# Kernel optimization log

Hardware: AMD Instinct MI355X
Metric: run time of the kernel (lower is better)

The kernel has to match this reference:

```python
import jax, jax.numpy as jnp
import numpy as np

B, T, C, H = 4, 1024, 1024, 16
HD = C // H
EPS = 1e-5


def _layernorm(x, w, b):
    mu = jnp.mean(x, axis=-1, keepdims=True)
    var = jnp.mean(jnp.square(x - mu), axis=-1, keepdims=True)
    return (x - mu) * jax.lax.rsqrt(var + EPS) * w + b


def setup_inputs() -> dict:
    key = jax.random.key(0)
    ks = jax.random.split(key, 10)
    s = 0.02
    return {
        "x": jax.random.normal(ks[0], (B, T, C), jnp.float32),
        "attention_mask": jnp.zeros((1, 1, T, T), jnp.float32),
        "ln1_w": jnp.ones((C,), jnp.float32),
        "ln1_b": jnp.zeros((C,), jnp.float32),
        "w_qkv": s * jax.random.normal(ks[1], (3 * C, C), jnp.float32),
        "b_qkv": jnp.zeros((3 * C,), jnp.float32),
        "w_o": s * jax.random.normal(ks[2], (C, C), jnp.float32),
        "b_o": jnp.zeros((C,), jnp.float32),
        "ln2_w": jnp.ones((C,), jnp.float32),
        "ln2_b": jnp.zeros((C,), jnp.float32),
        "w_fc": s * jax.random.normal(ks[3], (4 * C, C), jnp.float32),
        "b_fc": jnp.zeros((4 * C,), jnp.float32),
        "w_proj": s * jax.random.normal(ks[4], (C, 4 * C), jnp.float32),
        "b_proj": jnp.zeros((C,), jnp.float32),
    }


def reference(x, attention_mask, ln1_w, ln1_b, w_qkv, b_qkv, w_o, b_o,
              ln2_w, ln2_b, w_fc, b_fc, w_proj, b_proj):
    # --- self-attention on ln_1(x) ---
    h = _layernorm(x, ln1_w, ln1_b)
    qkv = h @ w_qkv.T + b_qkv                      # [B,T,3C]
    q, k, v = jnp.split(qkv, 3, axis=-1)
    q = q.reshape(B, T, H, HD).transpose(0, 2, 1, 3)  # [B,H,T,HD]
    k = k.reshape(B, T, H, HD).transpose(0, 2, 1, 3)
    v = v.reshape(B, T, H, HD).transpose(0, 2, 1, 3)
    att = jnp.einsum('bhqd,bhkd->bhqk', q, k) * (1.0 / np.sqrt(HD))
    att = att + attention_mask
    att_weights = jax.nn.softmax(att, axis=-1)     # [B,H,T,T]
    y = jnp.einsum('bhqk,bhkd->bhqd', att_weights, v)
    y = y.transpose(0, 2, 1, 3).reshape(B, T, C)
    y = y @ w_o.T + b_o
    x = x + y
    # --- MLP on ln_2(x), residual ---
    residual = x
    h2 = _layernorm(x, ln2_w, ln2_b)
    h2 = jax.nn.gelu(h2 @ w_fc.T + b_fc, approximate=False)
    h2 = h2 @ w_proj.T + b_proj
    x = residual + h2
    return (x, att_weights)
```

## Files before the change

### kernel.cpp

```cpp
#include <hip/hip_runtime.h>
#include <stdint.h>
#include <math.h>

typedef __attribute__((ext_vector_type(4))) float f32x4;
typedef __attribute__((ext_vector_type(8))) short s16x8;
typedef __attribute__((ext_vector_type(4))) unsigned short u16x4;
typedef __attribute__((ext_vector_type(8))) unsigned short u16x8;

__device__ __forceinline__ unsigned short f2b(float x) {
    union { float f; uint32_t u; } v; v.f = x;
    uint32_t r = v.u + 0x7FFFu + ((v.u >> 16) & 1u);
    return (unsigned short)(r >> 16);
}
__device__ __forceinline__ float b2f(unsigned short u) {
    union { uint32_t u; float f; } v; v.u = (uint32_t)u << 16;
    return v.f;
}

__device__ __forceinline__ void gload16(const unsigned short* g, unsigned short* l) {
    __builtin_amdgcn_global_load_lds(
        (const __attribute__((address_space(1))) unsigned int*)(const void*)g,
        (__attribute__((address_space(3))) unsigned int*)(void*)l,
        16, 0, 0);
}

__global__ __launch_bounds__(256) void cast4_kernel(
        const float* __restrict__ a, int na, const float* __restrict__ b, int nb,
        const float* __restrict__ c, int nc, const float* __restrict__ d, int nd,
        unsigned short* __restrict__ oa, unsigned short* __restrict__ ob,
        unsigned short* __restrict__ oc, unsigned short* __restrict__ od) {
    int i = blockIdx.x * 256 + threadIdx.x;
    const float* src; unsigned short* dst; int off;
    if (i < na)                { src = a; dst = oa; off = i; }
    else if (i < na+nb)        { src = b; dst = ob; off = i - na; }
    else if (i < na+nb+nc)     { src = c; dst = oc; off = i - na - nb; }
    else if (i < na+nb+nc+nd)  { src = d; dst = od; off = i - na - nb - nc; }
    else return;
    f32x4 v = ((const f32x4*)src)[off];
    u16x4 o;
    #pragma unroll
    for (int j = 0; j < 4; ++j) o[j] = f2b(v[j]);
    ((u16x4*)dst)[off] = o;
}

__global__ __launch_bounds__(256) void ln_kernel(const float* __restrict__ x,
                                                 const float* __restrict__ w,
                                                 const float* __restrict__ b,
                                                 unsigned short* __restrict__ out) {
    const long row = blockIdx.x;
    const int tid = threadIdx.x;
    f32x4 v = *(const f32x4*)(x + row * 1024 + tid * 4);
    float s  = v[0] + v[1] + v[2] + v[3];
    float sq = v[0]*v[0] + v[1]*v[1] + v[2]*v[2] + v[3]*v[3];
    #pragma unroll
    for (int off = 32; off; off >>= 1) {
        s  += __shfl_xor(s, off);
        sq += __shfl_xor(sq, off);
    }
    __shared__ float red[8];
    if ((tid & 63) == 0) { red[tid >> 6] = s; red[4 + (tid >> 6)] = sq; }
    __syncthreads();
    s  = red[0] + red[1] + red[2] + red[3];
    sq = red[4] + red[5] + red[6] + red[7];
    float mu  = s * (1.0f / 1024.0f);
    float var = sq * (1.0f / 1024.0f) - mu * mu;
    float rs  = rsqrtf(var + 1e-5f);
    f32x4 wv = *(const f32x4*)(w + tid * 4);
    f32x4 bv = *(const f32x4*)(b + tid * 4);
    u16x4 o;
    #pragma unroll
    for (int j = 0; j < 4; ++j) o[j] = f2b((v[j] - mu) * rs * wv[j] + bv[j]);
    *(u16x4*)(out + row * 1024 + tid * 4) = o;
}

__global__ __launch_bounds__(256) void inv_kernel(const float* __restrict__ psum,
                                                  float* __restrict__ invl) {
    const long r = blockIdx.x * 256 + threadIdx.x;
    const float* p = psum + (r << 4);
    f32x4 a = *(const f32x4*)p,       b = *(const f32x4*)(p + 4);
    f32x4 c = *(const f32x4*)(p + 8), d = *(const f32x4*)(p + 12);
    float s = (a[0]+a[1]+a[2]+a[3]) + (b[0]+b[1]+b[2]+b[3])
            + (c[0]+c[1]+c[2]+c[3]) + (d[0]+d[1]+d[2]+d[3]);
    invl[r] = 1.0f / s;
}

__global__ __launch_bounds__(256)
void pv_att(const unsigned short* __restrict__ E,
            const unsigned short* __restrict__ Vt,
            const float* __restrict__ invl,
            float* __restrict__ att,
            unsigned short* __restrict__ y) {
    __shared__ unsigned short ldsA[3][64 * 32];
    __shared__ unsigned short ldsB[3][64 * 32];
    const int tid = threadIdx.x, lane = tid & 63, wid = tid >> 6;
    const int wr = wid >> 1, wc = wid & 1;
    const int bh = blockIdx.y;
    const int q0 = blockIdx.x * 64;
    const int fr = lane & 15, fs = lane >> 4;

    const unsigned short* Ab = E + ((long)bh << 20) + (long)q0 * 1024;
    const unsigned short* Bb = Vt + ((long)bh << 16);

    const int e0  = wid * 512 + lane * 8;
    const int r0a = e0 >> 5, c0a = e0 & 31;
    const float il_a = invl[(bh << 10) + q0 + r0a];
    float* attRow = att + ((long)bh << 20) + (long)(q0 + r0a) * 1024 + c0a;

    f32x4 acc[2][2] = {};

#define PSTAGE(T, BUF)                                                        \
    {                                                                         \
        const int k0s = (T) << 5;                                             \
        gload16(Ab + k0s + (long)r0a * 1024 + c0a, &ldsA[BUF][wid * 512]);    \
        gload16(Bb + k0s + (long)r0a * 1024 + c0a, &ldsB[BUF][wid * 512]);    \
    }

    PSTAGE(0, 0);
    PSTAGE(1, 1);

    for (int t = 0; t < 32; ++t) {
        const int buf = t % 3;
        asm volatile("s_waitcnt vmcnt(4)" ::: "memory");
        __syncthreads();
        if (t + 2 < 32) PSTAGE(t + 2, (t + 2) % 3);

        {
            s16x8 ea = *(const s16x8*)&ldsA[buf][e0];
            f32x4 o0, o1;
            #pragma unroll
            for (int j = 0; j < 4; ++j) o0[j] = b2f((unsigned short)ea[j]) * il_a;
            #pragma unroll
            for (int j = 0; j < 4; ++j) o1[j] = b2f((unsigned short)ea[4 + j]) * il_a;
            *(f32x4*)(attRow + t * 32)     = o0;
            *(f32x4*)(attRow + t * 32 + 4) = o1;
        }

        s16x8 af[2], vb[2];
        #pragma unroll
        for (int m = 0; m < 2; ++m)
            af[m] = *(const s16x8*)&ldsA[buf][(wr * 32 + m * 16 + fr) * 32 + fs * 8];
        #pragma unroll
        for (int n = 0; n < 2; ++n)
            vb[n] = *(const s16x8*)&ldsB[buf][(wc * 32 + n * 16 + fr) * 32 + fs * 8];
        #pragma unroll
        for (int m = 0; m < 2; ++m)
            #pragma unroll
            for (int n = 0; n < 2; ++n)
                acc[m][n] = __builtin_amdgcn_mfma_f32_16x16x32_bf16(af[m], vb[n], acc[m][n], 0, 0, 0);
    }
#undef PSTAGE

    const int bb = bh >> 4, hh = bh & 15;
    #pragma unroll
    for (int m = 0; m < 2; ++m) {
        #pragma unroll
        for (int r = 0; r < 4; ++r) {
            const int trow = q0 + wr * 32 + m * 16 + fs * 4 + r;
            const float il = invl[(bh << 10) + trow];
            #pragma unroll
            for (int n = 0; n < 2; ++n) {
                const int c = hh * 64 + wc * 32 + n * 16 + fr;
                y[((long)(bb * 1024 + trow) << 10) + c] = f2b(acc[m][n][r] * il);
            }
        }
    }
}

template <int BM, int BN, int EPI>
__global__ __launch_bounds__(256)
void gemm_bt(const unsigned short* __restrict__ A,
             const unsigned short* __restrict__ Bm,
             int K, int lda, int ldb, int ldc,
             long sAz, long sBz,
             const float* __restrict__ bias,
             const float* __restrict__ resid,
             float* __restrict__ outF,
             unsigned short* __restrict__ outB) {
    constexpr int WM = BM / 2, WN = BN / 2;
    constexpr int FM = WM / 16, FN = WN / 16;
    constexpr int NTA = BM / 64, NTB = BN / 64;
    constexpr int LOADS = NTA + NTB;
    __shared__ unsigned short ldsA[3][BM * 32];
    __shared__ unsigned short ldsB[3][BN * 32];

    const int tid  = threadIdx.x;
    const int lane = tid & 63;
    const int wid  = tid >> 6;
    const int wr   = wid >> 1, wc = wid & 1;
    const int bz   = blockIdx.z;
    const int row0 = blockIdx.x * BM;
    const int col0 = blockIdx.y * BN;

    const unsigned short* Ab = A + (long)bz * sAz + (long)row0 * lda;
    const unsigned short* Bb = Bm + (long)bz * sBz + (long)col0 * ldb;

    const int nt = K >> 5;
    f32x4 acc[FM][FN] = {};
    const int fr = lane & 15;
    const int fk = (lane >> 4) * 8;

#define STAGE(T, BUF)                                                              \
    {                                                                              \
        const int k0s = (T) << 5;                                                  \
        _Pragma("unroll")                                                          \
        for (int i = 0; i < NTA; ++i) {                                            \
            int e = i * 2048 + wid * 512 + lane * 8;                               \
            gload16(Ab + k0s + (long)(e >> 5) * lda + (e & 31),                    \
                    &ldsA[BUF][i * 2048 + wid * 512]);                             \
        }                                                                          \
        _Pragma("unroll")                                                          \
        for (int i = 0; i < NTB; ++i) {                                            \
            int e = i * 2048 + wid * 512 + lane * 8;                               \
            gload16(Bb + k0s + (long)(e >> 5) * ldb + (e & 31),                    \
                    &ldsB[BUF][i * 2048 + wid * 512]);                             \
        }                                                                          \
    }

    STAGE(0, 0);
    if (nt > 1) STAGE(1, 1);

    for (int t = 0; t < nt; ++t) {
        const int buf = t % 3;
        if (t + 1 < nt) {
            if constexpr (LOADS == 2)      asm volatile("s_waitcnt vmcnt(2)" ::: "memory");
            else if constexpr (LOADS == 3) asm volatile("s_waitcnt vmcnt(3)" ::: "memory");
            else                           asm volatile("s_waitcnt vmcnt(4)" ::: "memory");
        } else {
            asm volatile("s_waitcnt vmcnt(0)" ::: "memory");
        }
        __syncthreads();
        if (t + 2 < nt) STAGE(t + 2, (t + 2) % 3);

        s16x8 af[FM], bfr[FN];
        #pragma unroll
        for (int m = 0; m < FM; ++m)
            af[m] = *(const s16x8*)&ldsA[buf][(wr * WM + m * 16 + fr) * 32 + fk];
        #pragma unroll
        for (int n = 0; n < FN; ++n)
            bfr[n] = *(const s16x8*)&ldsB[buf][(wc * WN + n * 16 + fr) * 32 + fk];
        #pragma unroll
        for (int m = 0; m < FM; ++m)
            #pragma unroll
            for (int n = 0; n < FN; ++n)
                acc[m][n] = __builtin_amdgcn_mfma_f32_16x16x32_bf16(af[m], bfr[n], acc[m][n], 0, 0, 0);
    }
#undef STAGE

    const int cj = lane & 15;
    const int r0 = (lane >> 4) * 4;

    if constexpr (EPI == 1) {
        #pragma unroll
        for (int m = 0; m < FM; ++m) {
            #pragma unroll
            for (int r = 0; r < 4; ++r) {
                const int grow = row0 + wr * WM + m * 16 + r0 + r;
                float rs = 0.0f;
                #pragma unroll
                for (int n = 0; n < FN; ++n) {
                    const int gcol = col0 + wc * WN + n * 16 + cj;
                    float e = __expf(acc[m][n][r] + resid[((long)grow << 10) + gcol]);
                    rs += e;
                    outB[((long)bz << 20) + ((long)grow << 10) + gcol] = f2b(e);
                }
                rs += __shfl_xor(rs, 1); rs += __shfl_xor(rs, 2);
                rs += __shfl_xor(rs, 4); rs += __shfl_xor(rs, 8);
                if (cj == 0)
                    outF[((((long)bz << 10) + grow) << 4) + blockIdx.y * 2 + wc] = rs;
            }
        }
    } else {
        #pragma unroll
        for (int m = 0; m < FM; ++m) {
            #pragma unroll
            for (int n = 0; n < FN; ++n) {
                #pragma unroll
                for (int r = 0; r < 4; ++r) {
                    const int grow = row0 + wr * WM + m * 16 + r0 + r;
                    const int gcol = col0 + wc * WN + n * 16 + cj;
                    float v = acc[m][n][r];
                    if constexpr (EPI == 0) {
                        v += bias[gcol];
                        const int bb = grow >> 10, t = grow & 1023;
                        const int seg = gcol >> 10, mm = gcol & 1023;
                        const int hh = mm >> 6, dd = mm & 63;
                        const long bh = bb * 16 + hh;
                        if (seg == 0)
                            outB[(bh << 16) + (t << 6) + dd] = f2b(v * 0.125f);
                        else if (seg == 1)
                            outB[4194304 + (bh << 16) + (t << 6) + dd] = f2b(v);
                        else
                            outB[8388608 + (bh << 16) + (dd << 10) + t] = f2b(v);
                    } else if constexpr (EPI == 3) {
                        const long idx = ((long)grow << 10) + gcol;
                        outF[idx] = v + bias[gcol] + resid[idx];
                    } else if constexpr (EPI == 4) {
                        float u = v + bias[gcol];
                        float g = 0.5f * u * (1.0f + erff(u * 0.70710678118f));
                        outB[(long)grow * ldc + gcol] = f2b(g);
                    }
                }
            }
        }
    }
}

extern "C" void kernel_launch(void* const* d_in, const int* in_sizes, int n_in,
                              void* d_out, int out_size, void* d_ws, size_t ws_size,
                              hipStream_t stream) {
    (void)in_sizes; (void)n_in; (void)out_size; (void)ws_size;
    const float* x     = (const float*)d_in[0];
    const float* mask  = (const float*)d_in[1];
    const float* ln1w  = (const float*)d_in[2];
    const float* ln1b  = (const float*)d_in[3];
    const float* wqkv  = (const float*)d_in[4];
    const float* bqkv  = (const float*)d_in[5];
    const float* wo    = (const float*)d_in[6];
    const float* bo    = (const float*)d_in[7];
    const float* ln2w  = (const float*)d_in[8];
    const float* ln2b  = (const float*)d_in[9];
    const float* wfc   = (const float*)d_in[10];
    const float* bfc   = (const float*)d_in[11];
    const float* wproj = (const float*)d_in[12];
    const float* bproj = (const float*)d_in[13];

    float* outx = (float*)d_out;
    float* att  = (float*)d_out + 4194304;

    char* ws = (char*)d_ws;
    unsigned short* h_bf     = (unsigned short*)ws;  ws += (size_t)8  << 20;
    unsigned short* wqkv_bf  = (unsigned short*)ws;  ws += (size_t)6  << 20;
    unsigned short* wo_bf    = (unsigned short*)ws;  ws += (size_t)2  << 20;
    unsigned short* wfc_bf   = (unsigned short*)ws;  ws += (size_t)8  << 20;
    unsigned short* wproj_bf = (unsigned short*)ws;  ws += (size_t)8  << 20;
    unsigned short* q_bf     = (unsigned short*)ws;  ws += (size_t)24 << 20;
    unsigned short* k_bf     = q_bf + 4194304;
    unsigned short* vT_bf    = q_bf + 8388608;
    unsigned short* e_b      = (unsigned short*)ws;  ws += (size_t)128 << 20;
    unsigned short* y_bf     = (unsigned short*)ws;  ws += (size_t)8  << 20;
    float*          x2       = (float*)ws;           ws += (size_t)16 << 20;
    unsigned short* gelu_bf  = (unsigned short*)ws;  ws += (size_t)32 << 20;
    float*          psum     = (float*)ws;           ws += (size_t)4  << 20;
    float*          invl     = (float*)ws;           ws += (size_t)256 << 10;

    cast4_kernel<<<12288, 256, 0, stream>>>(
        wqkv, 786432, wo, 262144, wfc, 1048576, wproj, 1048576,
        wqkv_bf, wo_bf, wfc_bf, wproj_bf);

    ln_kernel<<<4096, 256, 0, stream>>>(x, ln1w, ln1b, h_bf);

    gemm_bt<128, 128, 0><<<dim3(32, 24, 1), 256, 0, stream>>>(
        h_bf, wqkv_bf, 1024, 1024, 1024, 0, 0, 0,
        bqkv, nullptr, nullptr, q_bf);

    gemm_bt<128, 128, 1><<<dim3(8, 8, 64), 256, 0, stream>>>(
        q_bf, k_bf, 64, 64, 64, 0, 65536, 65536,
        nullptr, mask, psum, e_b);

    inv_kernel<<<256, 256, 0, stream>>>(psum, invl);

    pv_att<<<dim3(16, 64), 256, 0, stream>>>(e_b, vT_bf, invl, att, y_bf);

    gemm_bt<64, 128, 3><<<dim3(64, 8, 1), 256, 0, stream>>>(
        y_bf, wo_bf, 1024, 1024, 1024, 1024, 0, 0,
        bo, x, x2, nullptr);

    ln_kernel<<<4096, 256, 0, stream>>>(x2, ln2w, ln2b, h_bf);

    gemm_bt<128, 128, 4><<<dim3(32, 32, 1), 256, 0, stream>>>(
        h_bf, wfc_bf, 1024, 1024, 1024, 4096, 0, 0,
        bfc, nullptr, nullptr, gelu_bf);

    gemm_bt<64, 128, 3><<<dim3(64, 8, 1), 256, 0, stream>>>(
        gelu_bf, wproj_bf, 4096, 4096, 4096, 1024, 0, 0,
        bproj, x2, outx, nullptr);
}
```

Baseline: 448.9 us.

## Stage GEMM epilogues through LDS, fuse LN1 with weight cast, inline inverse sums

Several GEMM epilogues (QKV scatter, exp/softmax numerator, GELU) now write their results to shared memory and then store them back as 16-byte vectors, instead of scattering 2-byte elements. The QKV epilogue also performs the V transpose inside LDS. The first layernorm is merged into the weight-cast kernel, and the row-sum inversion kernel is folded into pv_att, which removes two launches. The pv_att wait count also changes. The extra LDS round trips and barriers add some cost, and the tighter vmcnt waits change how much loading overlaps with compute.

```diff
diff --git a/kernel.cpp b/kernel.cpp
--- a/kernel.cpp
+++ b/kernel.cpp
@@ -5,7 +5,6 @@
 typedef __attribute__((ext_vector_type(4))) float f32x4;
 typedef __attribute__((ext_vector_type(8))) short s16x8;
 typedef __attribute__((ext_vector_type(4))) unsigned short u16x4;
-typedef __attribute__((ext_vector_type(8))) unsigned short u16x8;
 
 __device__ __forceinline__ unsigned short f2b(float x) {
     union { float f; uint32_t u; } v; v.f = x;
@@ -24,23 +23,52 @@
         16, 0, 0);
 }
 
-__global__ __launch_bounds__(256) void cast4_kernel(
+__global__ __launch_bounds__(256) void castln_kernel(
+        const float* __restrict__ x, const float* __restrict__ lw,
+        const float* __restrict__ lb, unsigned short* __restrict__ lout,
         const float* __restrict__ a, int na, const float* __restrict__ b, int nb,
         const float* __restrict__ c, int nc, const float* __restrict__ d, int nd,
         unsigned short* __restrict__ oa, unsigned short* __restrict__ ob,
         unsigned short* __restrict__ oc, unsigned short* __restrict__ od) {
-    int i = blockIdx.x * 256 + threadIdx.x;
-    const float* src; unsigned short* dst; int off;
-    if (i < na)                { src = a; dst = oa; off = i; }
-    else if (i < na+nb)        { src = b; dst = ob; off = i - na; }
-    else if (i < na+nb+nc)     { src = c; dst = oc; off = i - na - nb; }
-    else if (i < na+nb+nc+nd)  { src = d; dst = od; off = i - na - nb - nc; }
-    else return;
-    f32x4 v = ((const f32x4*)src)[off];
-    u16x4 o;
-    #pragma unroll
-    for (int j = 0; j < 4; ++j) o[j] = f2b(v[j]);
-    ((u16x4*)dst)[off] = o;
+    const int tid = threadIdx.x;
+    if (blockIdx.x < 4096) {
+        const long row = blockIdx.x;
+        f32x4 v = *(const f32x4*)(x + row * 1024 + tid * 4);
+        float s  = v[0] + v[1] + v[2] + v[3];
+        float sq = v[0]*v[0] + v[1]*v[1] + v[2]*v[2] + v[3]*v[3];
+        #pragma unroll
+        for (int off = 32; off; off >>= 1) {
+            s  += __shfl_xor(s, off);
+            sq += __shfl_xor(sq, off);
+        }
+        __shared__ float red[8];
+        if ((tid & 63) == 0) { red[tid >> 6] = s; red[4 + (tid >> 6)] = sq; }
+        __syncthreads();
+        s  = red[0] + red[1] + red[2] + red[3];
+        sq = red[4] + red[5] + red[6] + red[7];
+        float mu  = s * (1.0f / 1024.0f);
+        float var = sq * (1.0f / 1024.0f) - mu * mu;
+        float rs  = rsqrtf(var + 1e-5f);
+        f32x4 wv = *(const f32x4*)(lw + tid * 4);
+        f32x4 bv = *(const f32x4*)(lb + tid * 4);
+        u16x4 o;
+        #pragma unroll
+        for (int j = 0; j < 4; ++j) o[j] = f2b((v[j] - mu) * rs * wv[j] + bv[j]);
+        *(u16x4*)(lout + row * 1024 + tid * 4) = o;
+    } else {
+        int i = (blockIdx.x - 4096) * 256 + tid;
+        const float* src; unsigned short* dst; int off;
+        if (i < na)                { src = a; dst = oa; off = i; }
+        else if (i < na+nb)        { src = b; dst = ob; off = i - na; }
+        else if (i < na+nb+nc)     { src = c; dst = oc; off = i - na - nb; }
+        else if (i < na+nb+nc+nd)  { src = d; dst = od; off = i - na - nb - nc; }
+        else return;
+        f32x4 v = ((const f32x4*)src)[off];
+        u16x4 o;
+        #pragma unroll
+        for (int j = 0; j < 4; ++j) o[j] = f2b(v[j]);
+        ((u16x4*)dst)[off] = o;
+    }
 }
 
 __global__ __launch_bounds__(256) void ln_kernel(const float* __restrict__ x,
@@ -73,25 +101,15 @@
     *(u16x4*)(out + row * 1024 + tid * 4) = o;
 }
 
-__global__ __launch_bounds__(256) void inv_kernel(const float* __restrict__ psum,
-                                                  float* __restrict__ invl) {
-    const long r = blockIdx.x * 256 + threadIdx.x;
-    const float* p = psum + (r << 4);
-    f32x4 a = *(const f32x4*)p,       b = *(const f32x4*)(p + 4);
-    f32x4 c = *(const f32x4*)(p + 8), d = *(const f32x4*)(p + 12);
-    float s = (a[0]+a[1]+a[2]+a[3]) + (b[0]+b[1]+b[2]+b[3])
-            + (c[0]+c[1]+c[2]+c[3]) + (d[0]+d[1]+d[2]+d[3]);
-    invl[r] = 1.0f / s;
-}
-
 __global__ __launch_bounds__(256)
 void pv_att(const unsigned short* __restrict__ E,
             const unsigned short* __restrict__ Vt,
-            const float* __restrict__ invl,
+            const float* __restrict__ psum,
             float* __restrict__ att,
             unsigned short* __restrict__ y) {
     __shared__ unsigned short ldsA[3][64 * 32];
     __shared__ unsigned short ldsB[3][64 * 32];
+    __shared__ float invl_s[64];
     const int tid = threadIdx.x, lane = tid & 63, wid = tid >> 6;
     const int wr = wid >> 1, wc = wid & 1;
     const int bh = blockIdx.y;
@@ -103,7 +121,6 @@
 
     const int e0  = wid * 512 + lane * 8;
     const int r0a = e0 >> 5, c0a = e0 & 31;
-    const float il_a = invl[(bh << 10) + q0 + r0a];
     float* attRow = att + ((long)bh << 20) + (long)(q0 + r0a) * 1024 + c0a;
 
     f32x4 acc[2][2] = {};
@@ -118,13 +135,24 @@
     PSTAGE(0, 0);
     PSTAGE(1, 1);
 
+    if (tid < 64) {
+        const float* p = psum + ((((long)bh << 10) + q0 + tid) << 4);
+        f32x4 pa = *(const f32x4*)p,       pb = *(const f32x4*)(p + 4);
+        f32x4 pc = *(const f32x4*)(p + 8), pd = *(const f32x4*)(p + 12);
+        float s = (pa[0]+pa[1]+pa[2]+pa[3]) + (pb[0]+pb[1]+pb[2]+pb[3])
+                + (pc[0]+pc[1]+pc[2]+pc[3]) + (pd[0]+pd[1]+pd[2]+pd[3]);
+        invl_s[tid] = 1.0f / s;
+    }
+
     for (int t = 0; t < 32; ++t) {
         const int buf = t % 3;
-        asm volatile("s_waitcnt vmcnt(4)" ::: "memory");
+        if (t < 31) asm volatile("s_waitcnt vmcnt(2)" ::: "memory");
+        else        asm volatile("s_waitcnt vmcnt(0)" ::: "memory");
         __syncthreads();
         if (t + 2 < 32) PSTAGE(t + 2, (t + 2) % 3);
 
         {
+            const float il_a = invl_s[r0a];
             s16x8 ea = *(const s16x8*)&ldsA[buf][e0];
             f32x4 o0, o1;
             #pragma unroll
@@ -155,8 +183,9 @@
     for (int m = 0; m < 2; ++m) {
         #pragma unroll
         for (int r = 0; r < 4; ++r) {
-            const int trow = q0 + wr * 32 + m * 16 + fs * 4 + r;
-            const float il = invl[(bh << 10) + trow];
+            const int lrow = wr * 32 + m * 16 + fs * 4 + r;
+            const float il = invl_s[lrow];
+            const int trow = q0 + lrow;
             #pragma unroll
             for (int n = 0; n < 2; ++n) {
                 const int c = hh * 64 + wc * 32 + n * 16 + fr;
@@ -180,8 +209,10 @@
     constexpr int FM = WM / 16, FN = WN / 16;
     constexpr int NTA = BM / 64, NTB = BN / 64;
     constexpr int LOADS = NTA + NTB;
-    __shared__ unsigned short ldsA[3][BM * 32];
-    __shared__ unsigned short ldsB[3][BN * 32];
+    constexpr int STR = 136;
+    __shared__ unsigned short shm[3 * BM * 32 + 3 * BN * 32];
+    unsigned short* ldsA = shm;
+    unsigned short* ldsB = shm + 3 * BM * 32;
 
     const int tid  = threadIdx.x;
     const int lane = tid & 63;
@@ -206,13 +237,13 @@
         for (int i = 0; i < NTA; ++i) {                                            \
             int e = i * 2048 + wid * 512 + lane * 8;                               \
             gload16(Ab + k0s + (long)(e >> 5) * lda + (e & 31),                    \
-                    &ldsA[BUF][i * 2048 + wid * 512]);                             \
+                    &ldsA[(BUF) * BM * 32 + i * 2048 + wid * 512]);                \
         }                                                                          \
         _Pragma("unroll")                                                          \
         for (int i = 0; i < NTB; ++i) {                                            \
             int e = i * 2048 + wid * 512 + lane * 8;                               \
             gload16(Bb + k0s + (long)(e >> 5) * ldb + (e & 31),                    \
-                    &ldsB[BUF][i * 2048 + wid * 512]);                             \
+                    &ldsB[(BUF) * BN * 32 + i * 2048 + wid * 512]);                \
         }                                                                          \
     }
 
@@ -234,10 +265,10 @@
         s16x8 af[FM], bfr[FN];
         #pragma unroll
         for (int m = 0; m < FM; ++m)
-            af[m] = *(const s16x8*)&ldsA[buf][(wr * WM + m * 16 + fr) * 32 + fk];
+            af[m] = *(const s16x8*)&ldsA[buf * BM * 32 + (wr * WM + m * 16 + fr) * 32 + fk];
         #pragma unroll
         for (int n = 0; n < FN; ++n)
-            bfr[n] = *(const s16x8*)&ldsB[buf][(wc * WN + n * 16 + fr) * 32 + fk];
+            bfr[n] = *(const s16x8*)&ldsB[buf * BN * 32 + (wc * WN + n * 16 + fr) * 32 + fk];
         #pragma unroll
         for (int m = 0; m < FM; ++m)
             #pragma unroll
@@ -250,18 +281,20 @@
     const int r0 = (lane >> 4) * 4;
 
     if constexpr (EPI == 1) {
+        __syncthreads();
         #pragma unroll
         for (int m = 0; m < FM; ++m) {
             #pragma unroll
             for (int r = 0; r < 4; ++r) {
-                const int grow = row0 + wr * WM + m * 16 + r0 + r;
+                const int prow = wr * WM + m * 16 + r0 + r;
+                const int grow = row0 + prow;
                 float rs = 0.0f;
                 #pragma unroll
                 for (int n = 0; n < FN; ++n) {
-                    const int gcol = col0 + wc * WN + n * 16 + cj;
-                    float e = __expf(acc[m][n][r] + resid[((long)grow << 10) + gcol]);
+                    const int pcol = wc * WN + n * 16 + cj;
+                    float e = __expf(acc[m][n][r] + resid[((long)grow << 10) + col0 + pcol]);
                     rs += e;
-                    outB[((long)bz << 20) + ((long)grow << 10) + gcol] = f2b(e);
+                    shm[prow * STR + pcol] = f2b(e);
                 }
                 rs += __shfl_xor(rs, 1); rs += __shfl_xor(rs, 2);
                 rs += __shfl_xor(rs, 4); rs += __shfl_xor(rs, 8);
@@ -269,6 +302,89 @@
                     outF[((((long)bz << 10) + grow) << 4) + blockIdx.y * 2 + wc] = rs;
             }
         }
+        __syncthreads();
+        #pragma unroll
+        for (int j = 0; j < 8; ++j) {
+            const int idx = j * 2048 + tid * 8;
+            const int row = idx >> 7, c = idx & 127;
+            s16x8 val = *(const s16x8*)&shm[row * STR + c];
+            *(s16x8*)(outB + ((long)bz << 20) + ((long)(row0 + row) << 10) + col0 + c) = val;
+        }
+    } else if constexpr (EPI == 0) {
+        const int seg = col0 >> 10;
+        const int bb = row0 >> 10;
+        __syncthreads();
+        if (seg < 2) {
+            #pragma unroll
+            for (int m = 0; m < FM; ++m)
+                #pragma unroll
+                for (int n = 0; n < FN; ++n)
+                    #pragma unroll
+                    for (int r = 0; r < 4; ++r) {
+                        const int prow = wr * WM + m * 16 + r0 + r;
+                        const int pcol = wc * WN + n * 16 + cj;
+                        float v = acc[m][n][r] + bias[col0 + pcol];
+                        if (seg == 0) v *= 0.125f;
+                        shm[prow * STR + pcol] = f2b(v);
+                    }
+            __syncthreads();
+            #pragma unroll
+            for (int j = 0; j < 8; ++j) {
+                const int idx = j * 2048 + tid * 8;
+                const int row = idx >> 7, c = idx & 127;
+                s16x8 val = *(const s16x8*)&shm[row * STR + c];
+                const int t = (row0 + row) & 1023;
+                const int hh = ((col0 & 1023) >> 6) + (c >> 6);
+                const int dd = c & 63;
+                const long bh = bb * 16 + hh;
+                *(s16x8*)(outB + (seg == 1 ? 4194304 : 0) + (bh << 16) + (t << 6) + dd) = val;
+            }
+        } else {
+            #pragma unroll
+            for (int m = 0; m < FM; ++m)
+                #pragma unroll
+                for (int n = 0; n < FN; ++n)
+                    #pragma unroll
+                    for (int r = 0; r < 4; ++r) {
+                        const int prow = wr * WM + m * 16 + r0 + r;
+                        const int pcol = wc * WN + n * 16 + cj;
+                        shm[pcol * 144 + prow] = f2b(acc[m][n][r] + bias[col0 + pcol]);
+                    }
+            __syncthreads();
+            #pragma unroll
+            for (int j = 0; j < 8; ++j) {
+                const int idx = j * 2048 + tid * 8;
+                const int ddl = idx >> 7, tl = idx & 127;
+                s16x8 val = *(const s16x8*)&shm[ddl * 144 + tl];
+                const int hh = ((col0 & 1023) >> 6) + (ddl >> 6);
+                const int dd = ddl & 63;
+                const int t = (row0 & 1023) + tl;
+                const long bh = bb * 16 + hh;
+                *(s16x8*)(outB + 8388608 + (bh << 16) + (dd << 10) + t) = val;
+            }
+        }
+    } else if constexpr (EPI == 4) {
+        __syncthreads();
+        #pragma unroll
+        for (int m = 0; m < FM; ++m)
+            #pragma unroll
+            for (int n = 0; n < FN; ++n)
+                #pragma unroll
+                for (int r = 0; r < 4; ++r) {
+                    const int prow = wr * WM + m * 16 + r0 + r;
+                    const int pcol = wc * WN + n * 16 + cj;
+                    float u = acc[m][n][r] + bias[col0 + pcol];
+                    float g = 0.5f * u * (1.0f + erff(u * 0.70710678118f));
+                    shm[prow * STR + pcol] = f2b(g);
+                }
+        __syncthreads();
+        #pragma unroll
+        for (int j = 0; j < 8; ++j) {
+            const int idx = j * 2048 + tid * 8;
+            const int row = idx >> 7, c = idx & 127;
+            s16x8 val = *(const s16x8*)&shm[row * STR + c];
+            *(s16x8*)(outB + (long)(row0 + row) * ldc + col0 + c) = val;
+        }
     } else {
         #pragma unroll
         for (int m = 0; m < FM; ++m) {
@@ -278,27 +394,8 @@
                 for (int r = 0; r < 4; ++r) {
                     const int grow = row0 + wr * WM + m * 16 + r0 + r;
                     const int gcol = col0 + wc * WN + n * 16 + cj;
-                    float v = acc[m][n][r];
-                    if constexpr (EPI == 0) {
-                        v += bias[gcol];
-                        const int bb = grow >> 10, t = grow & 1023;
-                        const int seg = gcol >> 10, mm = gcol & 1023;
-                        const int hh = mm >> 6, dd = mm & 63;
-                        const long bh = bb * 16 + hh;
-                        if (seg == 0)
-                            outB[(bh << 16) + (t << 6) + dd] = f2b(v * 0.125f);
-                        else if (seg == 1)
-                            outB[4194304 + (bh << 16) + (t << 6) + dd] = f2b(v);
-                        else
-                            outB[8388608 + (bh << 16) + (dd << 10) + t] = f2b(v);
-                    } else if constexpr (EPI == 3) {
-                        const long idx = ((long)grow << 10) + gcol;
-                        outF[idx] = v + bias[gcol] + resid[idx];
-                    } else if constexpr (EPI == 4) {
-                        float u = v + bias[gcol];
-                        float g = 0.5f * u * (1.0f + erff(u * 0.70710678118f));
-                        outB[(long)grow * ldc + gcol] = f2b(g);
-                    }
+                    const long idx = ((long)grow << 10) + gcol;
+                    outF[idx] = acc[m][n][r] + bias[gcol] + resid[idx];
                 }
             }
         }
@@ -341,13 +438,11 @@
     float*          x2       = (float*)ws;           ws += (size_t)16 << 20;
     unsigned short* gelu_bf  = (unsigned short*)ws;  ws += (size_t)32 << 20;
     float*          psum     = (float*)ws;           ws += (size_t)4  << 20;
-    float*          invl     = (float*)ws;           ws += (size_t)256 << 10;
-
-    cast4_kernel<<<12288, 256, 0, stream>>>(
+
+    castln_kernel<<<16384, 256, 0, stream>>>(
+        x, ln1w, ln1b, h_bf,
         wqkv, 786432, wo, 262144, wfc, 1048576, wproj, 1048576,
         wqkv_bf, wo_bf, wfc_bf, wproj_bf);
-
-    ln_kernel<<<4096, 256, 0, stream>>>(x, ln1w, ln1b, h_bf);
 
     gemm_bt<128, 128, 0><<<dim3(32, 24, 1), 256, 0, stream>>>(
         h_bf, wqkv_bf, 1024, 1024, 1024, 0, 0, 0,
@@ -357,9 +452,7 @@
         q_bf, k_bf, 64, 64, 64, 0, 65536, 65536,
         nullptr, mask, psum, e_b);
 
-    inv_kernel<<<256, 256, 0, stream>>>(psum, invl);
-
-    pv_att<<<dim3(16, 64), 256, 0, stream>>>(e_b, vT_bf, invl, att, y_bf);
+    pv_att<<<dim3(16, 64), 256, 0, stream>>>(e_b, vT_bf, psum, att, y_bf);
 
     gemm_bt<64, 128, 3><<<dim3(64, 8, 1), 256, 0, stream>>>(
         y_bf, wo_bf, 1024, 1024, 1024, 1024, 0, 0,
```

Result: faster. 423.9 us (-5.6%).
